# Performance work log

Hardware: AMD Instinct MI355X
Metric: run time of the kernel (lower is better)

## Reference

```python
import jax, jax.numpy as jnp
import numpy as np

N_NODES = 50000
N_EDGES = 800000
F_IN = 128
HID = 128
N_CLASSES = 16
SELF_LOOP_W = 2.0  # improved=True -> self-loop fill value 2.0


def _glorot(key, fan_in, fan_out):
    scale = jnp.sqrt(6.0 / (fan_in + fan_out))
    return jax.random.uniform(key, (fan_in, fan_out), jnp.float32, -scale, scale)


def gcn_conv(x, W, b, src, dst, n):
    # PyG GCNConv (improved): out = D^{-1/2} (A + 2I) D^{-1/2} (x W) + b
    h = x @ W                                   # [N, F_out] dense transform
    deg = jnp.zeros((n,), x.dtype).at[dst].add(1.0) + SELF_LOOP_W  # in-degree + 2
    dinv = jax.lax.rsqrt(deg)                   # deg^{-1/2}
    norm = dinv[src] * dinv[dst]                # per-edge coefficient [E]
    msg = h[src] * norm[:, None]                # gather + scale [E, F_out]
    agg = jax.ops.segment_sum(msg, dst, num_segments=n)
    agg = agg + (SELF_LOOP_W * dinv * dinv)[:, None] * h  # self-loop term
    return agg + b


def setup_inputs() -> dict:
    key = jax.random.key(0)
    ks = jax.random.split(key, 10)
    x = jax.random.normal(ks[0], (N_NODES, F_IN), jnp.float32)
    edge_index = jax.random.randint(ks[1], (2, N_EDGES), 0, N_NODES, jnp.int64)
    return {
        "x": x,
        "edge_index": edge_index,
        "W0": _glorot(ks[2], F_IN, HID), "b0": jnp.zeros((HID,), jnp.float32),
        "W1": _glorot(ks[3], HID, HID),  "b1": jnp.zeros((HID,), jnp.float32),
        "W2": _glorot(ks[4], HID, HID),  "b2": jnp.zeros((HID,), jnp.float32),
        "W3": _glorot(ks[5], HID, N_CLASSES), "b3": jnp.zeros((N_CLASSES,), jnp.float32),
    }


def reference(x, edge_index, W0, b0, W1, b1, W2, b2, W3, b3):
    src, dst = edge_index[0], edge_index[1]
    # dropout is identity in eval mode
    h = jax.nn.relu(gcn_conv(x, W0, b0, src, dst, N_NODES))
    h = jax.nn.relu(gcn_conv(h, W1, b1, src, dst, N_NODES))
    h = jax.nn.relu(gcn_conv(h, W2, b2, src, dst, N_NODES))
    return jnp.tanh(gcn_conv(h, W3, b3, src, dst, N_NODES))
```

## Files before the change

kernel.cpp:

```cpp
#include <hip/hip_runtime.h>
#include <hip/hip_fp16.h>
#include <math.h>

#define N_NODES 50000
#define N_EDGES 800000
#define NB 782
#define CH 4096
#define CAP 2048
#define BUCKET_BLOCKS 196
#define CAST_BLOCKS 6250
#define PREPW_BLOCKS 192
#define W3_BLOCKS 8
#define BPREP_GRID (BUCKET_BLOCKS + CAST_BLOCKS + PREPW_BLOCKS + W3_BLOCKS)
#define FB 1563

typedef _Float16 half8 __attribute__((ext_vector_type(8)));
typedef float floatx4 __attribute__((ext_vector_type(4)));
typedef unsigned uintx4 __attribute__((ext_vector_type(4)));

__global__ __launch_bounds__(256) void k_bucket_prep(
    const int* __restrict__ src, const int* __restrict__ dst,
    int* __restrict__ gcur, unsigned* __restrict__ arena,
    const float* __restrict__ x, __half* __restrict__ xh,
    const float* __restrict__ W0, const float* __restrict__ W1,
    const float* __restrict__ W2, const float* __restrict__ W3,
    __half* __restrict__ WT, __half* __restrict__ WT3) {
    const int t = threadIdx.x;
    if (blockIdx.x >= BUCKET_BLOCKS) {
        int xb = blockIdx.x - BUCKET_BLOCKS;
        if (xb < CAST_BLOCKS) {
            int i = xb * 256 + t;
            float4 v = *(const float4*)&x[(size_t)i * 4];
            union { ushort4 u; __half h[4]; } p;
            p.h[0] = __float2half(v.x); p.h[1] = __float2half(v.y);
            p.h[2] = __float2half(v.z); p.h[3] = __float2half(v.w);
            *(ushort4*)&xh[(size_t)i * 4] = p.u;
        } else {
            int idx = xb - CAST_BLOCKS;
            if (idx < PREPW_BLOCKS) {
                int which = idx >> 6;
                const float* W = (which == 0) ? W0 : (which == 1) ? W1 : W2;
                int i = (idx & 63) * 256 + t;
                int k = i >> 7, n = i & 127;
                int np = ((n & 7) << 4) + (n >> 3);
                WT[which * 128 * 128 + np * 128 + k] = __float2half(W[i]);
            } else {
                int i = (idx - PREPW_BLOCKS) * 256 + t;
                int n = i >> 7, k = i & 127;
                WT3[n * 128 + k] = __float2half(W3[k * 16 + n]);
            }
        }
        return;
    }
    __shared__ int cntA[NB];
    __shared__ int lofs[NB];
    __shared__ int gbase[NB];
    __shared__ int part[256];
    __shared__ unsigned buf[CH];
    const int ebase = blockIdx.x * CH;
    const int chunkN = min(CH, N_EDGES - ebase);

    for (int i = t; i < NB; i += 256) cntA[i] = 0;
    __syncthreads();
    for (int i = t; i < chunkN; i += 256)
        atomicAdd(&cntA[dst[ebase + i] >> 6], 1);
    __syncthreads();
    int c[4];
    int s = 0;
#pragma unroll
    for (int q = 0; q < 4; ++q) {
        int idx = t * 4 + q;
        c[q] = (idx < NB) ? cntA[idx] : 0;
        s += c[q];
    }
    part[t] = s;
    __syncthreads();
    for (int d = 1; d < 256; d <<= 1) {
        int u = (t >= d) ? part[t - d] : 0;
        __syncthreads();
        part[t] += u;
        __syncthreads();
    }
    int run = (t > 0) ? part[t - 1] : 0;
#pragma unroll
    for (int q = 0; q < 4; ++q) {
        int idx = t * 4 + q;
        if (idx < NB) {
            lofs[idx] = run;
            run += c[q];
            gbase[idx] = (c[q] > 0) ? atomicAdd(&gcur[idx], c[q]) : 0;
            cntA[idx] = 0;
        }
    }
    __syncthreads();
    for (int i = t; i < chunkN; i += 256) {
        int d = dst[ebase + i];
        int sv = src[ebase + i];
        int b = d >> 6;
        int pos = atomicAdd(&cntA[b], 1);
        buf[lofs[b] + pos] = ((unsigned)d << 16) | (unsigned)sv;
    }
    __syncthreads();
    for (int i = t; i < chunkN; i += 256) {
        unsigned v = buf[i];
        int b = (int)(v >> 16) >> 6;
        int q = i - lofs[b];
        int p = gbase[b] + q;
        if (p < CAP) arena[((size_t)b << 11) + p] = v;
    }
}

__global__ __launch_bounds__(256) void k_fill(
    const unsigned* __restrict__ arena, const int* __restrict__ gcur,
    unsigned* __restrict__ packed, float* __restrict__ dinv,
    unsigned short* __restrict__ eidx) {
    const int t = threadIdx.x;
    const int b = blockIdx.x;
    __shared__ int cnt64[64];
    __shared__ int cur64[64];
    if (t < 64) cnt64[t] = 0;
    __syncthreads();
    const int seglen = min(gcur[b], CAP);
    const unsigned* seg = arena + ((size_t)b << 11);
    for (int i = t; i < seglen; i += 256)
        atomicAdd(&cnt64[(seg[i] >> 16) & 63], 1);
    __syncthreads();
    if (t < 64) {
        int v = cnt64[t];
        int p = v;
#pragma unroll
        for (int d = 1; d < 64; d <<= 1) {
            int u = __shfl_up(p, d, 64);
            if (t >= d) p += u;
        }
        int excl = p - v;
        int node = b * 64 + t;
        if (node < N_NODES) {
            packed[node] = ((unsigned)((b << 11) + excl) << 11) | (unsigned)v;
            dinv[node] = rsqrtf((float)v + 2.0f);
        }
        cur64[t] = excl;
    }
    __syncthreads();
    const int base = b << 11;
    for (int i = t; i < seglen; i += 256) {
        unsigned v = seg[i];
        int d = (int)(v >> 16) & 63;
        int pos = atomicAdd(&cur64[d], 1);
        eidx[base + pos] = (unsigned short)(v & 0xFFFFu);
    }
}

__device__ __forceinline__ void accs(uint4 ua, uint4 ub, float s, float* acc) {
    union { uint4 u; __half2 h2[4]; } va, vb;
    va.u = ua; vb.u = ub;
#pragma unroll
    for (int q = 0; q < 4; ++q) {
        float2 wa = __half22float2(va.h2[q]);
        float2 wb = __half22float2(vb.h2[q]);
        acc[2 * q]     += s * wa.x;
        acc[2 * q + 1] += s * wa.y;
        acc[8 + 2 * q]     += s * wb.x;
        acc[8 + 2 * q + 1] += s * wb.y;
    }
}

template <bool SC>
__device__ __forceinline__ void gather_stage(
    int r, bool valid, int l8, const __half* __restrict__ pin,
    const float* __restrict__ dinv, const unsigned* __restrict__ packed,
    const unsigned short* __restrict__ eidx, float* acc) {
#pragma unroll
    for (int j = 0; j < 16; ++j) acc[j] = 0.f;
    int i = 0, end = 0;
    if (valid) {
        const uint4* rp = (const uint4*)&pin[(size_t)r * 128];
        uint4 sa = rp[l8], sb = rp[8 + l8];
        float s2 = SC ? 2.f * dinv[r] : 2.f;
        accs(sa, sb, s2, acc);
        unsigned pk = packed[r];
        i = (int)(pk >> 11);
        end = i + (int)(pk & 2047u);
    }
    for (; i + 8 <= end; i += 8) {
        int my = (int)eidx[i + l8];
        uint4 va[8], vb[8];
        float ds8[8];
#pragma unroll
        for (int j = 0; j < 8; ++j) {
            int s0 = __shfl(my, j, 8);
            const uint4* q = (const uint4*)&pin[(size_t)s0 * 128];
            va[j] = q[l8];
            vb[j] = q[8 + l8];
            if (SC) ds8[j] = dinv[s0];
        }
#pragma unroll
        for (int j = 0; j < 8; ++j)
            accs(va[j], vb[j], SC ? ds8[j] : 1.f, acc);
    }
    if (i < end) {
        int n = end - i;
        int my = (l8 < n) ? (int)eidx[i + l8] : 0;
        for (int j = 0; j < n; ++j) {
            int s0 = __shfl(my, j, 8);
            const uint4* q = (const uint4*)&pin[(size_t)s0 * 128];
            accs(q[l8], q[8 + l8], SC ? dinv[s0] : 1.f, acc);
        }
    }
}

template <bool SC>
__global__ __launch_bounds__(256, 2) void k_fused(
    const __half* __restrict__ pin, const __half* __restrict__ WTl,
    const float* __restrict__ dinv, const unsigned* __restrict__ packed,
    const unsigned short* __restrict__ eidx, const float* __restrict__ bias,
    __half* __restrict__ pout) {
    __shared__ __half tl[32 * 136];
    const int t = threadIdx.x;
    const int node8 = t >> 3;
    const int l8 = t & 7;
    const int r = blockIdx.x * 32 + node8;

    float acc[16];
    gather_stage<SC>(r, r < N_NODES, l8, pin, dinv, packed, eidx, acc);

    {
        union { uintx4 u; __half h[8]; } pa, pb;
#pragma unroll
        for (int j = 0; j < 8; ++j) {
            pa.h[j] = __float2half(acc[j]);
            pb.h[j] = __float2half(acc[8 + j]);
        }
        *(uintx4*)&tl[node8 * 136 + 8 * l8] = pa.u;
        *(uintx4*)&tl[node8 * 136 + 64 + 8 * l8] = pb.u;
    }
    __syncthreads();

    const int wave = t >> 6;
    const int lane = t & 63;
    const int m = lane & 15;
    const int quad = lane >> 4;
    const int rtile = wave >> 1;
    const int ctile = wave & 1;
    floatx4 a4[4] = {};
#pragma unroll
    for (int kb = 0; kb < 4; ++kb) {
        half8 af = *(const half8*)&tl[(rtile * 16 + m) * 136 + quad * 8 + kb * 32];
#pragma unroll
        for (int j = 0; j < 4; ++j) {
            half8 bf = *(const half8*)&WTl[(size_t)(((ctile * 4 + j) * 16 + m)) * 128 +
                                           kb * 32 + quad * 8];
            a4[j] = __builtin_amdgcn_mfma_f32_16x16x32_f16(af, bf, a4[j], 0, 0, 0);
        }
    }
    const int f0 = 8 * m + ctile * 4;
    const float4 bi = *(const float4*)&bias[f0];
    const int nb0 = blockIdx.x * 32 + rtile * 16 + quad * 4;
#pragma unroll
    for (int rr = 0; rr < 4; ++rr) {
        int node = nb0 + rr;
        if (node < N_NODES) {
            float dv = dinv[node];
            union { ushort4 u; __half h[4]; } pk4;
            pk4.h[0] = __float2half(fmaxf(dv * (dv * a4[0][rr] + bi.x), 0.f));
            pk4.h[1] = __float2half(fmaxf(dv * (dv * a4[1][rr] + bi.y), 0.f));
            pk4.h[2] = __float2half(fmaxf(dv * (dv * a4[2][rr] + bi.z), 0.f));
            pk4.h[3] = __float2half(fmaxf(dv * (dv * a4[3][rr] + bi.w), 0.f));
            *(ushort4*)&pout[(size_t)node * 128 + f0] = pk4.u;
        }
    }
}

__global__ __launch_bounds__(256, 2) void k_fused_last(
    const __half* __restrict__ pin, const __half* __restrict__ WTl,
    const __half* __restrict__ WT3, const float* __restrict__ dinv,
    const unsigned* __restrict__ packed, const unsigned short* __restrict__ eidx,
    const float* __restrict__ bias, float* __restrict__ H16) {
    __shared__ __half tl[32 * 136];
    const int t = threadIdx.x;
    const int node8 = t >> 3;
    const int l8 = t & 7;
    const int r = blockIdx.x * 32 + node8;

    float acc[16];
    gather_stage<false>(r, r < N_NODES, l8, pin, dinv, packed, eidx, acc);

    {
        union { uintx4 u; __half h[8]; } pa, pb;
#pragma unroll
        for (int j = 0; j < 8; ++j) {
            pa.h[j] = __float2half(acc[j]);
            pb.h[j] = __float2half(acc[8 + j]);
        }
        *(uintx4*)&tl[node8 * 136 + 8 * l8] = pa.u;
        *(uintx4*)&tl[node8 * 136 + 64 + 8 * l8] = pb.u;
    }
    __syncthreads();

    const int wave = t >> 6;
    const int lane = t & 63;
    const int m = lane & 15;
    const int quad = lane >> 4;
    const int rtile = wave >> 1;
    const int ctile = wave & 1;
    floatx4 a4[4] = {};
#pragma unroll
    for (int kb = 0; kb < 4; ++kb) {
        half8 af = *(const half8*)&tl[(rtile * 16 + m) * 136 + quad * 8 + kb * 32];
#pragma unroll
        for (int j = 0; j < 4; ++j) {
            half8 bf = *(const half8*)&WTl[(size_t)(((ctile * 4 + j) * 16 + m)) * 128 +
                                           kb * 32 + quad * 8];
            a4[j] = __builtin_amdgcn_mfma_f32_16x16x32_f16(af, bf, a4[j], 0, 0, 0);
        }
    }
    __syncthreads();

    const int f0 = 8 * m + ctile * 4;
    const float4 bi = *(const float4*)&bias[f0];
    const int rowb = rtile * 16 + quad * 4;
#pragma unroll
    for (int rr = 0; rr < 4; ++rr) {
        int node = blockIdx.x * 32 + rowb + rr;
        float dv = (node < N_NODES) ? dinv[node] : 0.f;
        union { ushort4 u; __half h[4]; } pk4;
        pk4.h[0] = __float2half(fmaxf(dv * (dv * a4[0][rr] + bi.x), 0.f));
        pk4.h[1] = __float2half(fmaxf(dv * (dv * a4[1][rr] + bi.y), 0.f));
        pk4.h[2] = __float2half(fmaxf(dv * (dv * a4[2][rr] + bi.z), 0.f));
        pk4.h[3] = __float2half(fmaxf(dv * (dv * a4[3][rr] + bi.w), 0.f));
        *(ushort4*)&tl[(rowb + rr) * 136 + f0] = pk4.u;
    }
    __syncthreads();

    if (wave < 2) {
        floatx4 c2 = {};
#pragma unroll
        for (int kb = 0; kb < 4; ++kb) {
            half8 af2 = *(const half8*)&tl[(wave * 16 + m) * 136 + quad * 8 + kb * 32];
            half8 bf2 = *(const half8*)&WT3[(size_t)m * 128 + kb * 32 + quad * 8];
            c2 = __builtin_amdgcn_mfma_f32_16x16x32_f16(af2, bf2, c2, 0, 0, 0);
        }
#pragma unroll
        for (int rr = 0; rr < 4; ++rr) {
            int node = blockIdx.x * 32 + wave * 16 + quad * 4 + rr;
            if (node < N_NODES) H16[(size_t)node * 16 + m] = c2[rr];
        }
    }
}

__global__ __launch_bounds__(256) void k_gather4(const unsigned* __restrict__ packed,
                                                 const unsigned short* __restrict__ eidx,
                                                 const float* __restrict__ hs,
                                                 const float* __restrict__ dinv,
                                                 const float* __restrict__ bias,
                                                 float* __restrict__ out) {
    int tid = blockIdx.x * 256 + threadIdx.x;
    int r = tid >> 2;
    if (r >= N_NODES) return;
    int l = tid & 3;
    int f = l * 4;
    const float dv = dinv[r];
    const float4 bi = *(const float4*)&bias[f];
    float4 h = *(const float4*)&hs[(size_t)r * 16 + f];
    float ax = 2.f * h.x, ay = 2.f * h.y, az = 2.f * h.z, aw = 2.f * h.w;
    unsigned pk = packed[r];
    int i = (int)(pk >> 11);
    int end = i + (int)(pk & 2047u);
    for (; i + 4 <= end; i += 4) {
        int my = (int)eidx[i + l];
#pragma unroll
        for (int j = 0; j < 4; ++j) {
            int s = __shfl(my, j, 4);
            float4 v = *(const float4*)&hs[(size_t)s * 16 + f];
            ax += v.x; ay += v.y; az += v.z; aw += v.w;
        }
    }
    if (i < end) {
        int n = end - i;
        int my = (l < n) ? (int)eidx[i + l] : 0;
        for (int j = 0; j < n; ++j) {
            int s = __shfl(my, j, 4);
            float4 v = *(const float4*)&hs[(size_t)s * 16 + f];
            ax += v.x; ay += v.y; az += v.z; aw += v.w;
        }
    }
    float v0 = tanhf(dv * ax + bi.x);
    float v1 = tanhf(dv * ay + bi.y);
    float v2 = tanhf(dv * az + bi.z);
    float v3 = tanhf(dv * aw + bi.w);
    floatx4 o = {v0, v1, v2, v3};
    __builtin_nontemporal_store(o, (floatx4*)&out[(size_t)r * 16 + f]);
}

extern "C" void kernel_launch(void* const* d_in, const int* in_sizes, int n_in,
                              void* d_out, int out_size, void* d_ws, size_t ws_size,
                              hipStream_t stream) {
    const float* x  = (const float*)d_in[0];
    const int* ei   = (const int*)d_in[1];
    const float* W0 = (const float*)d_in[2];
    const float* b0 = (const float*)d_in[3];
    const float* W1 = (const float*)d_in[4];
    const float* b1 = (const float*)d_in[5];
    const float* W2 = (const float*)d_in[6];
    const float* b2 = (const float*)d_in[7];
    const float* W3 = (const float*)d_in[8];
    const float* b3 = (const float*)d_in[9];
    const int* src = ei;
    const int* dst = ei + N_EDGES;

    __half* A      = (__half*)d_ws;
    __half* P      = A + (size_t)N_NODES * 128;
    __half* WT     = P + (size_t)N_NODES * 128;
    __half* WT3    = WT + 3 * 128 * 128;
    float*  H16    = (float*)(WT3 + 16 * 128);
    float*  dinv   = H16 + (size_t)N_NODES * 16;
    unsigned* packed = (unsigned*)(dinv + N_NODES);
    int*    gcur   = (int*)(packed + N_NODES);
    unsigned short* eidx = (unsigned short*)(gcur + 1024);
    unsigned* arena = (unsigned*)(eidx + NB * CAP);

    (void)hipMemsetAsync(gcur, 0, 1024 * sizeof(int), stream);
    k_bucket_prep<<<BPREP_GRID, 256, 0, stream>>>(src, dst, gcur, arena, x, A,
                                                  W0, W1, W2, W3, WT, WT3);
    k_fill<<<NB, 256, 0, stream>>>(arena, gcur, packed, dinv, eidx);

    k_fused<true><<<FB, 256, 0, stream>>>(A, WT, dinv, packed, eidx, b0, P);
    k_fused<false><<<FB, 256, 0, stream>>>(P, WT + 128 * 128, dinv, packed,
                                           eidx, b1, A);
    k_fused_last<<<FB, 256, 0, stream>>>(A, WT + 2 * 128 * 128, WT3, dinv,
                                         packed, eidx, b2, H16);
    k_gather4<<<(N_NODES * 4 + 255) / 256, 256, 0, stream>>>(
        packed, eidx, H16, dinv, b3, (float*)d_out);
}
```

Before: 255.0 us.

## Build CSR with global degree atomics, block scan and atomic placement

Replaces the shared-memory bucketed arena build (bucket kernel plus per-bucket fill kernel) with a three-step CSR construction. Node degrees are counted with global atomics inside the prep kernel, a scan kernel computes each node's global offset and dinv with wave shuffles and one atomic per block, and a place kernel writes each edge's source into its slot with a per-node atomic cursor. This drops the fixed-capacity arena and its two-level staging, at the cost of two rounds of random global atomics and scattered 2-byte writes to eidx.

```diff
diff --git a/kernel.cpp b/kernel.cpp
--- a/kernel.cpp
+++ b/kernel.cpp
@@ -4,151 +4,101 @@
 
 #define N_NODES 50000
 #define N_EDGES 800000
-#define NB 782
-#define CH 4096
-#define CAP 2048
-#define BUCKET_BLOCKS 196
+#define DEG_BLOCKS 782
 #define CAST_BLOCKS 6250
 #define PREPW_BLOCKS 192
 #define W3_BLOCKS 8
-#define BPREP_GRID (BUCKET_BLOCKS + CAST_BLOCKS + PREPW_BLOCKS + W3_BLOCKS)
+#define PREP0_GRID (DEG_BLOCKS + CAST_BLOCKS + PREPW_BLOCKS + W3_BLOCKS)
+#define SCAN_BLOCKS 196
+#define PLACE_BLOCKS 3125
 #define FB 1563
 
 typedef _Float16 half8 __attribute__((ext_vector_type(8)));
 typedef float floatx4 __attribute__((ext_vector_type(4)));
 typedef unsigned uintx4 __attribute__((ext_vector_type(4)));
 
-__global__ __launch_bounds__(256) void k_bucket_prep(
-    const int* __restrict__ src, const int* __restrict__ dst,
-    int* __restrict__ gcur, unsigned* __restrict__ arena,
+__global__ __launch_bounds__(256) void k_prep0(
+    const int* __restrict__ dst, unsigned* __restrict__ deg,
     const float* __restrict__ x, __half* __restrict__ xh,
     const float* __restrict__ W0, const float* __restrict__ W1,
     const float* __restrict__ W2, const float* __restrict__ W3,
     __half* __restrict__ WT, __half* __restrict__ WT3) {
     const int t = threadIdx.x;
-    if (blockIdx.x >= BUCKET_BLOCKS) {
-        int xb = blockIdx.x - BUCKET_BLOCKS;
-        if (xb < CAST_BLOCKS) {
-            int i = xb * 256 + t;
-            float4 v = *(const float4*)&x[(size_t)i * 4];
-            union { ushort4 u; __half h[4]; } p;
-            p.h[0] = __float2half(v.x); p.h[1] = __float2half(v.y);
-            p.h[2] = __float2half(v.z); p.h[3] = __float2half(v.w);
-            *(ushort4*)&xh[(size_t)i * 4] = p.u;
+    if (blockIdx.x < DEG_BLOCKS) {
+        int i4 = blockIdx.x * 256 + t;
+        if (i4 < N_EDGES / 4) {
+            int4 d4 = *(const int4*)&dst[i4 * 4];
+            atomicAdd(&deg[d4.x], 1u);
+            atomicAdd(&deg[d4.y], 1u);
+            atomicAdd(&deg[d4.z], 1u);
+            atomicAdd(&deg[d4.w], 1u);
+        }
+        return;
+    }
+    int xb = blockIdx.x - DEG_BLOCKS;
+    if (xb < CAST_BLOCKS) {
+        int i = xb * 256 + t;
+        float4 v = *(const float4*)&x[(size_t)i * 4];
+        union { ushort4 u; __half h[4]; } p;
+        p.h[0] = __float2half(v.x); p.h[1] = __float2half(v.y);
+        p.h[2] = __float2half(v.z); p.h[3] = __float2half(v.w);
+        *(ushort4*)&xh[(size_t)i * 4] = p.u;
+    } else {
+        int idx = xb - CAST_BLOCKS;
+        if (idx < PREPW_BLOCKS) {
+            int which = idx >> 6;
+            const float* W = (which == 0) ? W0 : (which == 1) ? W1 : W2;
+            int i = (idx & 63) * 256 + t;
+            int k = i >> 7, n = i & 127;
+            int np = ((n & 7) << 4) + (n >> 3);
+            WT[which * 128 * 128 + np * 128 + k] = __float2half(W[i]);
         } else {
-            int idx = xb - CAST_BLOCKS;
-            if (idx < PREPW_BLOCKS) {
-                int which = idx >> 6;
-                const float* W = (which == 0) ? W0 : (which == 1) ? W1 : W2;
-                int i = (idx & 63) * 256 + t;
-                int k = i >> 7, n = i & 127;
-                int np = ((n & 7) << 4) + (n >> 3);
-                WT[which * 128 * 128 + np * 128 + k] = __float2half(W[i]);
-            } else {
-                int i = (idx - PREPW_BLOCKS) * 256 + t;
-                int n = i >> 7, k = i & 127;
-                WT3[n * 128 + k] = __float2half(W3[k * 16 + n]);
-            }
-        }
-        return;
-    }
-    __shared__ int cntA[NB];
-    __shared__ int lofs[NB];
-    __shared__ int gbase[NB];
-    __shared__ int part[256];
-    __shared__ unsigned buf[CH];
-    const int ebase = blockIdx.x * CH;
-    const int chunkN = min(CH, N_EDGES - ebase);
-
-    for (int i = t; i < NB; i += 256) cntA[i] = 0;
-    __syncthreads();
-    for (int i = t; i < chunkN; i += 256)
-        atomicAdd(&cntA[dst[ebase + i] >> 6], 1);
-    __syncthreads();
-    int c[4];
-    int s = 0;
-#pragma unroll
-    for (int q = 0; q < 4; ++q) {
-        int idx = t * 4 + q;
-        c[q] = (idx < NB) ? cntA[idx] : 0;
-        s += c[q];
-    }
-    part[t] = s;
-    __syncthreads();
-    for (int d = 1; d < 256; d <<= 1) {
-        int u = (t >= d) ? part[t - d] : 0;
-        __syncthreads();
-        part[t] += u;
-        __syncthreads();
-    }
-    int run = (t > 0) ? part[t - 1] : 0;
-#pragma unroll
-    for (int q = 0; q < 4; ++q) {
-        int idx = t * 4 + q;
-        if (idx < NB) {
-            lofs[idx] = run;
-            run += c[q];
-            gbase[idx] = (c[q] > 0) ? atomicAdd(&gcur[idx], c[q]) : 0;
-            cntA[idx] = 0;
-        }
-    }
-    __syncthreads();
-    for (int i = t; i < chunkN; i += 256) {
-        int d = dst[ebase + i];
-        int sv = src[ebase + i];
-        int b = d >> 6;
-        int pos = atomicAdd(&cntA[b], 1);
-        buf[lofs[b] + pos] = ((unsigned)d << 16) | (unsigned)sv;
-    }
-    __syncthreads();
-    for (int i = t; i < chunkN; i += 256) {
-        unsigned v = buf[i];
-        int b = (int)(v >> 16) >> 6;
-        int q = i - lofs[b];
-        int p = gbase[b] + q;
-        if (p < CAP) arena[((size_t)b << 11) + p] = v;
-    }
-}
-
-__global__ __launch_bounds__(256) void k_fill(
-    const unsigned* __restrict__ arena, const int* __restrict__ gcur,
+            int i = (idx - PREPW_BLOCKS) * 256 + t;
+            int n = i >> 7, k = i & 127;
+            WT3[n * 128 + k] = __float2half(W3[k * 16 + n]);
+        }
+    }
+}
+
+__global__ __launch_bounds__(256) void k_scan(
+    const unsigned* __restrict__ deg, unsigned* __restrict__ gtotal,
     unsigned* __restrict__ packed, float* __restrict__ dinv,
-    unsigned short* __restrict__ eidx) {
+    unsigned* __restrict__ cursor) {
+    __shared__ unsigned wsum[4];
+    __shared__ unsigned bbase;
     const int t = threadIdx.x;
-    const int b = blockIdx.x;
-    __shared__ int cnt64[64];
-    __shared__ int cur64[64];
-    if (t < 64) cnt64[t] = 0;
-    __syncthreads();
-    const int seglen = min(gcur[b], CAP);
-    const unsigned* seg = arena + ((size_t)b << 11);
-    for (int i = t; i < seglen; i += 256)
-        atomicAdd(&cnt64[(seg[i] >> 16) & 63], 1);
-    __syncthreads();
-    if (t < 64) {
-        int v = cnt64[t];
-        int p = v;
-#pragma unroll
-        for (int d = 1; d < 64; d <<= 1) {
-            int u = __shfl_up(p, d, 64);
-            if (t >= d) p += u;
-        }
-        int excl = p - v;
-        int node = b * 64 + t;
-        if (node < N_NODES) {
-            packed[node] = ((unsigned)((b << 11) + excl) << 11) | (unsigned)v;
-            dinv[node] = rsqrtf((float)v + 2.0f);
-        }
-        cur64[t] = excl;
-    }
-    __syncthreads();
-    const int base = b << 11;
-    for (int i = t; i < seglen; i += 256) {
-        unsigned v = seg[i];
-        int d = (int)(v >> 16) & 63;
-        int pos = atomicAdd(&cur64[d], 1);
-        eidx[base + pos] = (unsigned short)(v & 0xFFFFu);
-    }
+    const int node = blockIdx.x * 256 + t;
+    unsigned d = (node < N_NODES) ? deg[node] : 0u;
+    unsigned p = d;
+#pragma unroll
+    for (int off = 1; off < 64; off <<= 1) {
+        unsigned u = __shfl_up(p, off, 64);
+        if ((t & 63) >= off) p += u;
+    }
+    if ((t & 63) == 63) wsum[t >> 6] = p;
+    __syncthreads();
+    if (t == 0) {
+        unsigned s0 = wsum[0], s1 = wsum[1], s2 = wsum[2], s3 = wsum[3];
+        bbase = atomicAdd(gtotal, s0 + s1 + s2 + s3);
+        wsum[0] = 0; wsum[1] = s0; wsum[2] = s0 + s1; wsum[3] = s0 + s1 + s2;
+    }
+    __syncthreads();
+    unsigned excl = bbase + wsum[t >> 6] + p - d;
+    if (node < N_NODES) {
+        packed[node] = (excl << 11) | d;
+        dinv[node] = rsqrtf((float)d + 2.0f);
+        cursor[node] = excl;
+    }
+}
+
+__global__ __launch_bounds__(256) void k_place(
+    const int* __restrict__ src, const int* __restrict__ dst,
+    unsigned* __restrict__ cursor, unsigned short* __restrict__ eidx) {
+    int e = blockIdx.x * 256 + threadIdx.x;
+    int d = dst[e];
+    int s = src[e];
+    unsigned pos = atomicAdd(&cursor[d], 1u);
+    eidx[pos] = (unsigned short)s;
 }
 
 __device__ __forceinline__ void accs(uint4 ua, uint4 ub, float s, float* acc) {
@@ -415,14 +365,16 @@
     float*  H16    = (float*)(WT3 + 16 * 128);
     float*  dinv   = H16 + (size_t)N_NODES * 16;
     unsigned* packed = (unsigned*)(dinv + N_NODES);
-    int*    gcur   = (int*)(packed + N_NODES);
-    unsigned short* eidx = (unsigned short*)(gcur + 1024);
-    unsigned* arena = (unsigned*)(eidx + NB * CAP);
-
-    (void)hipMemsetAsync(gcur, 0, 1024 * sizeof(int), stream);
-    k_bucket_prep<<<BPREP_GRID, 256, 0, stream>>>(src, dst, gcur, arena, x, A,
-                                                  W0, W1, W2, W3, WT, WT3);
-    k_fill<<<NB, 256, 0, stream>>>(arena, gcur, packed, dinv, eidx);
+    unsigned* deg  = packed + N_NODES;
+    unsigned* gtot = deg + N_NODES;
+    unsigned* cursor = gtot + 4;
+    unsigned short* eidx = (unsigned short*)(cursor + N_NODES);
+
+    (void)hipMemsetAsync(deg, 0, (N_NODES + 4) * sizeof(unsigned), stream);
+    k_prep0<<<PREP0_GRID, 256, 0, stream>>>(dst, deg, x, A, W0, W1, W2, W3,
+                                            WT, WT3);
+    k_scan<<<SCAN_BLOCKS, 256, 0, stream>>>(deg, gtot, packed, dinv, cursor);
+    k_place<<<PLACE_BLOCKS, 256, 0, stream>>>(src, dst, cursor, eidx);
 
     k_fused<true><<<FB, 256, 0, stream>>>(A, WT, dinv, packed, eidx, b0, P);
     k_fused<false><<<FB, 256, 0, stream>>>(P, WT + 128 * 128, dinv, packed,
```

Result: slower. 301.3 us (+18.2%).
